# Performance work log

Measured on AMD Instinct MI355X. Metric: run time of the kernel, lower is better.

## Reference

```python
import jax, jax.numpy as jnp
import numpy as np

B, C, D, H, W = 16, 64, 16, 48, 48
R = 4  # SE reduction ratio -> hidden = C // R = 16
NEG_SLOPE = 0.01  # torch nn.LeakyReLU default


def setup_inputs() -> dict:
    key = jax.random.key(0)
    k_x, k_w1, k_b1, k_w2, k_b2 = jax.random.split(key, 5)
    hid = C // R
    x = jax.random.normal(k_x, (B, C, D, H, W), dtype=jnp.float32)
    # 1x1 Conv2d weights act as per-channel linear maps: [out_ch, in_ch]
    w1 = jax.random.normal(k_w1, (hid, C), dtype=jnp.float32) * (1.0 / np.sqrt(C))
    b1 = jnp.zeros((hid,), dtype=jnp.float32)
    w2 = jax.random.normal(k_w2, (C, hid), dtype=jnp.float32) * (1.0 / np.sqrt(hid))
    b2 = jnp.zeros((C,), dtype=jnp.float32)
    return {"x": x, "w1": w1, "b1": b1, "w2": w2, "b2": b2}


def _leaky_relu(v):
    return jnp.where(v >= 0, v, NEG_SLOPE * v)


def reference(x, w1, b1, w2, b2):
    # Global average pool over spatial dims: [B, C, D]
    pooled = x.mean(axis=(3, 4))
    # SE gate: 1x1 convs over channel dim C (D acts as a spatial axis)
    h = jnp.einsum('bcd,oc->bod', pooled, w1) + b1[None, :, None]
    h = _leaky_relu(h)
    gate = jax.nn.sigmoid(jnp.einsum('bhd,oh->bod', h, w2) + b2[None, :, None])  # [B, C, D]
    # Broadcast multiply (replaces the original triple python loop)
    return x * gate[:, :, :, None, None]
```

## Files before the change

kernel.cpp:

```cpp
#include <hip/hip_runtime.h>

#define BB 16
#define CC 64
#define DD 16
#define HW 2304
#define HID 16
#define NEG_SLOPE 0.01f
#define CH4 9216

using f4 = __attribute__((ext_vector_type(4))) float;

__device__ __forceinline__ uint2 pack_bf16x4(f4 v) {
    uint2 r;
    asm("v_cvt_pk_bf16_f32 %0, %1, %2" : "=v"(r.x) : "v"(v.x), "v"(v.y));
    asm("v_cvt_pk_bf16_f32 %0, %1, %2" : "=v"(r.y) : "v"(v.z), "v"(v.w));
    return r;
}

__device__ __forceinline__ f4 unpack_mul(uint2 p, float g) {
    f4 v;
    v.x = __uint_as_float(p.x << 16) * g;
    v.y = __uint_as_float(p.x & 0xffff0000u) * g;
    v.z = __uint_as_float(p.y << 16) * g;
    v.w = __uint_as_float(p.y & 0xffff0000u) * g;
    return v;
}

__global__ __launch_bounds__(1024) void fused_se_kernel(
    const float* __restrict__ x,
    const float* __restrict__ w1, const float* __restrict__ b1,
    const float* __restrict__ w2, const float* __restrict__ b2,
    float* __restrict__ out)
{
    const int bd   = blockIdx.x;
    const int b    = bd >> 4;
    const int d    = bd & 15;
    const int tid  = threadIdx.x;
    const int wave = tid >> 6;
    const int lane = tid & 63;

    __shared__ uint2 stage[19][1024];
    __shared__ float pooled[CC];
    __shared__ float hbuf[HID];
    __shared__ float gate_s[CC];

    const size_t base4 = ((size_t)(b * CC) * DD + d) * (HW / 4);
    const f4* xb = (const f4*)x + base4 + lane;

    uint2 rv[17];

    #pragma unroll
    for (int i = 0; i < 4; ++i) {
        const f4* p = xb + (size_t)(wave * 4 + i) * CH4;
        const int nreg  = (i == 0) ? 5 : 4;
        const int rbase = (i == 0) ? 0 : 5 + (i - 1) * 4;
        const int lbase = (i == 0) ? 0 : 4 + (i - 1) * 5;
        float s = 0.f;
        #pragma unroll
        for (int j = 0; j < 9; ++j) {
            f4 v = p[j * 64];
            s += (v.x + v.y) + (v.z + v.w);
            uint2 pk = pack_bf16x4(v);
            if (j < nreg) rv[rbase + j] = pk;
            else          stage[lbase + (j - nreg)][tid] = pk;
        }
        #pragma unroll
        for (int m = 32; m; m >>= 1) s += __shfl_xor(s, m, 64);
        if (lane == 0) pooled[wave * 4 + i] = s * (1.0f / HW);
    }
    __syncthreads();

    {
        float v = w1[wave * CC + lane] * pooled[lane];
        #pragma unroll
        for (int m = 32; m; m >>= 1) v += __shfl_xor(v, m, 64);
        if (lane == 0) {
            float acc = v + b1[wave];
            hbuf[wave] = acc >= 0.f ? acc : NEG_SLOPE * acc;
        }
    }
    __syncthreads();
    if (tid < CC) {
        float acc = b2[tid];
        #pragma unroll
        for (int o = 0; o < HID; ++o) acc += w2[tid * HID + o] * hbuf[o];
        gate_s[tid] = 1.0f / (1.0f + expf(-acc));
    }
    __syncthreads();

    f4* ob = (f4*)out + base4 + lane;
    #pragma unroll
    for (int i = 0; i < 4; ++i) {
        const float gv = gate_s[wave * 4 + i];
        f4* q = ob + (size_t)(wave * 4 + i) * CH4;
        const int nreg  = (i == 0) ? 5 : 4;
        const int rbase = (i == 0) ? 0 : 5 + (i - 1) * 4;
        const int lbase = (i == 0) ? 0 : 4 + (i - 1) * 5;
        #pragma unroll
        for (int j = 0; j < 9; ++j) {
            uint2 pk = (j < nreg) ? rv[rbase + j] : stage[lbase + (j - nreg)][tid];
            __builtin_nontemporal_store(unpack_mul(pk, gv), q + j * 64);
        }
    }
}

extern "C" void kernel_launch(void* const* d_in, const int* in_sizes, int n_in,
                              void* d_out, int out_size, void* d_ws, size_t ws_size,
                              hipStream_t stream) {
    const float* x  = (const float*)d_in[0];
    const float* w1 = (const float*)d_in[1];
    const float* b1 = (const float*)d_in[2];
    const float* w2 = (const float*)d_in[3];
    const float* b2 = (const float*)d_in[4];
    float* out = (float*)d_out;

    fused_se_kernel<<<BB * DD, 1024, 0, stream>>>(x, w1, b1, w2, b2, out);
}
```

Measured before the change: 53.45 us.

## Split each slice across two blocks with inter-block pooled-sum exchange via flags

Each (b,d) slice is now handled by two 1024-thread blocks, each covering 32 channels, so 512 blocks run instead of 256. Every value a thread keeps sits in registers, which removes the LDS staging buffer. The two blocks pass their partial pooled sums through a global workspace and spin on an atomic counter, and a separate launch zeroes the counters first. The extra parallelism and occupancy come at the cost of a second kernel launch and a spin-wait that assumes both blocks of a pair are co-resident.

```diff
diff --git a/kernel.cpp b/kernel.cpp
--- a/kernel.cpp
+++ b/kernel.cpp
@@ -7,6 +7,8 @@
 #define HID 16
 #define NEG_SLOPE 0.01f
 #define CH4 9216
+#define NSLICE 256
+#define NBLK 512
 
 using f4 = __attribute__((ext_vector_type(4))) float;
 
@@ -26,52 +28,70 @@
     return v;
 }
 
-__global__ __launch_bounds__(1024) void fused_se_kernel(
+__global__ void zero_flags_kernel(unsigned* __restrict__ flags) {
+    if (threadIdx.x < NSLICE) flags[threadIdx.x] = 0u;
+}
+
+__global__ __launch_bounds__(1024, 8) void fused_se_kernel(
     const float* __restrict__ x,
     const float* __restrict__ w1, const float* __restrict__ b1,
     const float* __restrict__ w2, const float* __restrict__ b2,
-    float* __restrict__ out)
+    float* __restrict__ out,
+    float* __restrict__ pool_ws, unsigned* __restrict__ flags)
 {
-    const int bd   = blockIdx.x;
-    const int b    = bd >> 4;
-    const int d    = bd & 15;
-    const int tid  = threadIdx.x;
-    const int wave = tid >> 6;
-    const int lane = tid & 63;
+    const int g     = blockIdx.x;
+    const int slice = g >> 1;
+    const int half  = g & 1;
+    const int b = slice >> 4, d = slice & 15;
+    const int tid = threadIdx.x, wave = tid >> 6, lane = tid & 63;
+    const int cbase = half * 32;
+    const int c0 = cbase + wave * 2;
 
-    __shared__ uint2 stage[19][1024];
-    __shared__ float pooled[CC];
+    __shared__ float pooled_all[CC];
     __shared__ float hbuf[HID];
-    __shared__ float gate_s[CC];
+    __shared__ float gate_s[32];
 
     const size_t base4 = ((size_t)(b * CC) * DD + d) * (HW / 4);
-    const f4* xb = (const f4*)x + base4 + lane;
 
-    uint2 rv[17];
+    uint2 rv[18];
 
     #pragma unroll
-    for (int i = 0; i < 4; ++i) {
-        const f4* p = xb + (size_t)(wave * 4 + i) * CH4;
-        const int nreg  = (i == 0) ? 5 : 4;
-        const int rbase = (i == 0) ? 0 : 5 + (i - 1) * 4;
-        const int lbase = (i == 0) ? 0 : 4 + (i - 1) * 5;
+    for (int ch = 0; ch < 2; ++ch) {
+        const f4* p = (const f4*)x + base4 + (size_t)(c0 + ch) * CH4 + lane;
         float s = 0.f;
         #pragma unroll
         for (int j = 0; j < 9; ++j) {
             f4 v = p[j * 64];
             s += (v.x + v.y) + (v.z + v.w);
-            uint2 pk = pack_bf16x4(v);
-            if (j < nreg) rv[rbase + j] = pk;
-            else          stage[lbase + (j - nreg)][tid] = pk;
+            rv[ch * 9 + j] = pack_bf16x4(v);
         }
         #pragma unroll
         for (int m = 32; m; m >>= 1) s += __shfl_xor(s, m, 64);
-        if (lane == 0) pooled[wave * 4 + i] = s * (1.0f / HW);
+        if (lane == 0) pooled_all[c0 + ch] = s * (1.0f / HW);
     }
     __syncthreads();
 
+    if (tid < 32) {
+        __hip_atomic_store(&pool_ws[slice * CC + cbase + tid],
+                           pooled_all[cbase + tid],
+                           __ATOMIC_RELAXED, __HIP_MEMORY_SCOPE_AGENT);
+        __hip_atomic_fetch_add(&flags[slice], 1u,
+                               __ATOMIC_RELEASE, __HIP_MEMORY_SCOPE_AGENT);
+    }
+    if (tid == 0) {
+        while (__hip_atomic_load(&flags[slice], __ATOMIC_ACQUIRE,
+                                 __HIP_MEMORY_SCOPE_AGENT) < 64u)
+            __builtin_amdgcn_s_sleep(2);
+    }
+    __syncthreads();
+    if (tid < CC)
+        pooled_all[tid] = __hip_atomic_load(&pool_ws[slice * CC + tid],
+                                            __ATOMIC_RELAXED,
+                                            __HIP_MEMORY_SCOPE_AGENT);
+    __syncthreads();
+
     {
-        float v = w1[wave * CC + lane] * pooled[lane];
+        float v = w1[wave * CC + lane] * pooled_all[lane];
         #pragma unroll
         for (int m = 32; m; m >>= 1) v += __shfl_xor(v, m, 64);
         if (lane == 0) {
@@ -80,27 +100,22 @@
         }
     }
     __syncthreads();
-    if (tid < CC) {
-        float acc = b2[tid];
+    if (tid < 32) {
+        const int c = cbase + tid;
+        float acc = b2[c];
         #pragma unroll
-        for (int o = 0; o < HID; ++o) acc += w2[tid * HID + o] * hbuf[o];
+        for (int o = 0; o < HID; ++o) acc += w2[c * HID + o] * hbuf[o];
         gate_s[tid] = 1.0f / (1.0f + expf(-acc));
     }
     __syncthreads();
 
-    f4* ob = (f4*)out + base4 + lane;
     #pragma unroll
-    for (int i = 0; i < 4; ++i) {
-        const float gv = gate_s[wave * 4 + i];
-        f4* q = ob + (size_t)(wave * 4 + i) * CH4;
-        const int nreg  = (i == 0) ? 5 : 4;
-        const int rbase = (i == 0) ? 0 : 5 + (i - 1) * 4;
-        const int lbase = (i == 0) ? 0 : 4 + (i - 1) * 5;
+    for (int ch = 0; ch < 2; ++ch) {
+        const float gv = gate_s[wave * 2 + ch];
+        f4* q = (f4*)out + base4 + (size_t)(c0 + ch) * CH4 + lane;
         #pragma unroll
-        for (int j = 0; j < 9; ++j) {
-            uint2 pk = (j < nreg) ? rv[rbase + j] : stage[lbase + (j - nreg)][tid];
-            __builtin_nontemporal_store(unpack_mul(pk, gv), q + j * 64);
-        }
+        for (int j = 0; j < 9; ++j)
+            __builtin_nontemporal_store(unpack_mul(rv[ch * 9 + j], gv), q + j * 64);
     }
 }
 
@@ -114,5 +129,10 @@
     const float* b2 = (const float*)d_in[4];
     float* out = (float*)d_out;
 
-    fused_se_kernel<<<BB * DD, 1024, 0, stream>>>(x, w1, b1, w2, b2, out);
+    unsigned* flags = (unsigned*)d_ws;
+    float* pool_ws  = (float*)((char*)d_ws + 1024);
+
+    zero_flags_kernel<<<1, 256, 0, stream>>>(flags);
+    fused_se_kernel<<<NBLK, 1024, 0, stream>>>(x, w1, b1, w2, b2, out,
+                                               pool_ws, flags);
 }
```

Result: slower. 73.68 us (+37.8%).

## Shrink LDS staging and re-read part of input from global to raise occupancy

Applied to the files above, without the earlier changes.

Reduces the shared-memory staging buffer from 19 to 9 slots and keeps 18 packed entries in registers. The remaining chunks per channel are re-loaded from global memory during the output phase instead of being cached on chip. Lower LDS use is meant to allow more than one 1024-thread block per CU so pooling and writeback of different blocks can overlap. The cost is extra global reads, which depend on cache hits, plus possible register pressure under the tightened launch bounds.

```diff
diff --git a/kernel.cpp b/kernel.cpp
--- a/kernel.cpp
+++ b/kernel.cpp
@@ -26,7 +26,17 @@
     return v;
 }
 
-__global__ __launch_bounds__(1024) void fused_se_kernel(
+__device__ __forceinline__ f4 gmul(f4 v, float g) {
+    v.x *= g; v.y *= g; v.z *= g; v.w *= g;
+    return v;
+}
+
+__device__ constexpr int RC[4]    = {5, 5, 4, 4};
+__device__ constexpr int LC[4]    = {2, 2, 3, 2};
+__device__ constexpr int RBASE[4] = {0, 5, 10, 14};
+__device__ constexpr int LBASE[4] = {0, 2, 4, 7};
+
+__global__ __launch_bounds__(1024, 8) void fused_se_kernel(
     const float* __restrict__ x,
     const float* __restrict__ w1, const float* __restrict__ b1,
     const float* __restrict__ w2, const float* __restrict__ b2,
@@ -39,7 +49,7 @@
     const int wave = tid >> 6;
     const int lane = tid & 63;
 
-    __shared__ uint2 stage[19][1024];
+    __shared__ uint2 stage[9][1024];
     __shared__ float pooled[CC];
     __shared__ float hbuf[HID];
     __shared__ float gate_s[CC];
@@ -47,22 +57,18 @@
     const size_t base4 = ((size_t)(b * CC) * DD + d) * (HW / 4);
     const f4* xb = (const f4*)x + base4 + lane;
 
-    uint2 rv[17];
+    uint2 rv[18];
 
     #pragma unroll
     for (int i = 0; i < 4; ++i) {
         const f4* p = xb + (size_t)(wave * 4 + i) * CH4;
-        const int nreg  = (i == 0) ? 5 : 4;
-        const int rbase = (i == 0) ? 0 : 5 + (i - 1) * 4;
-        const int lbase = (i == 0) ? 0 : 4 + (i - 1) * 5;
         float s = 0.f;
         #pragma unroll
         for (int j = 0; j < 9; ++j) {
             f4 v = p[j * 64];
             s += (v.x + v.y) + (v.z + v.w);
-            uint2 pk = pack_bf16x4(v);
-            if (j < nreg) rv[rbase + j] = pk;
-            else          stage[lbase + (j - nreg)][tid] = pk;
+            if (j < RC[i])              rv[RBASE[i] + j] = pack_bf16x4(v);
+            else if (j < RC[i] + LC[i]) stage[LBASE[i] + j - RC[i]][tid] = pack_bf16x4(v);
         }
         #pragma unroll
         for (int m = 32; m; m >>= 1) s += __shfl_xor(s, m, 64);
@@ -92,15 +98,26 @@
     #pragma unroll
     for (int i = 0; i < 4; ++i) {
         const float gv = gate_s[wave * 4 + i];
-        f4* q = ob + (size_t)(wave * 4 + i) * CH4;
-        const int nreg  = (i == 0) ? 5 : 4;
-        const int rbase = (i == 0) ? 0 : 5 + (i - 1) * 4;
-        const int lbase = (i == 0) ? 0 : 4 + (i - 1) * 5;
+        const f4* p = xb + (size_t)(wave * 4 + i) * CH4;
+        f4*       q = ob + (size_t)(wave * 4 + i) * CH4;
+
+        f4 rr[3];
+        const int nrr = 9 - RC[i] - LC[i];
+        #pragma unroll
+        for (int k = 0; k < 3; ++k)
+            if (k < nrr) rr[k] = p[(RC[i] + LC[i] + k) * 64];
+
         #pragma unroll
         for (int j = 0; j < 9; ++j) {
-            uint2 pk = (j < nreg) ? rv[rbase + j] : stage[lbase + (j - nreg)][tid];
-            __builtin_nontemporal_store(unpack_mul(pk, gv), q + j * 64);
+            if (j < RC[i])
+                __builtin_nontemporal_store(unpack_mul(rv[RBASE[i] + j], gv), q + j * 64);
+            else if (j < RC[i] + LC[i])
+                __builtin_nontemporal_store(unpack_mul(stage[LBASE[i] + j - RC[i]][tid], gv), q + j * 64);
         }
+        #pragma unroll
+        for (int k = 0; k < 3; ++k)
+            if (k < nrr)
+                __builtin_nontemporal_store(gmul(rr[k], gv), q + (RC[i] + LC[i] + k) * 64);
     }
 }
 
```

Result: slower. 55.71 us (+4.2%).
